# Kernel tuning notes

Hardware: AMD Instinct MI355X
Metric: run time of the kernel (lower is better)

The kernel has to match this reference:

```python
import jax, jax.numpy as jnp
import numpy as np

WEIGHT = 0.1  # HISCLoss weight


def _gram(X):
    # linear kernel (the module's 'rbf' branch computes X @ Y.T)
    X = X.reshape(X.shape[0], -1)
    return X @ X.T  # [B, B]


def _center(K):
    # H K H with H = I - 11^T/B  ==  K - rowmean - colmean + grandmean
    rm = K.mean(axis=1, keepdims=True)
    cm = K.mean(axis=0, keepdims=True)
    gm = K.mean()
    return K - rm - cm + gm


def _hsic(X, Y):
    B = X.shape[0]
    Kc = _center(_gram(X))
    Lc = _center(_gram(Y))
    # trace(Kc @ Lc) without the B^3 matmul
    tr = jnp.einsum('ij,ji->', Kc, Lc)
    return tr / ((B - 1) ** 2)


def setup_inputs() -> dict:
    key = jax.random.key(0)
    ks = jax.random.split(key, 4)
    B, d = 4096, 256
    return {
        'e0': jax.random.normal(ks[0], (B, d), dtype=jnp.float32),
        'e1': jax.random.normal(ks[1], (B, d), dtype=jnp.float32),
        'e2': jax.random.normal(ks[2], (B, d), dtype=jnp.float32),
        'e3': jax.random.normal(ks[3], (B, d), dtype=jnp.float32),
    }


def reference(e0, e1, e2, e3):
    experts = [e0, e1, e2, e3]
    n = len(experts)
    vals = []
    for i in range(n):
        for j in range(i + 1, n):
            vals.append(_hsic(experts[i], experts[j]))
    L_hsic = jnp.mean(jnp.stack(vals))
    return WEIGHT * L_hsic
```

## Files before the change

### kernel.cpp

```cpp
#include <hip/hip_runtime.h>
#include <hip/hip_bf16.h>

#define B_ROWS 4096
#define DIM 256
#define NPAIR 6
#define PITCH 4160
#define BK 256
#define KSPLIT 8
#define KCHUNK (B_ROWS / KSPLIT)

typedef short bf16x8 __attribute__((ext_vector_type(8)));
typedef float f32x4 __attribute__((ext_vector_type(4)));

__device__ __forceinline__ const float* sel(const float* e0, const float* e1,
                                            const float* e2, const float* e3, int i) {
    return i == 0 ? e0 : (i == 1 ? e1 : (i == 2 ? e2 : e3));
}

__device__ __forceinline__ int pair_i(int p) { return p < 3 ? 0 : (p < 5 ? 1 : 2); }
__device__ __forceinline__ int pair_j(int p) { return p < 3 ? p + 1 : (p < 5 ? p - 1 : 3); }

__device__ __forceinline__ unsigned short f32_to_bf16_rne(float f) {
    unsigned int u = __float_as_uint(f);
    unsigned int r = (u + 0x7FFFu + ((u >> 16) & 1u)) >> 16;
    return (unsigned short)r;
}

__device__ __forceinline__ void glds16(const void* g, void* l) {
    __builtin_amdgcn_global_load_lds(
        (const __attribute__((address_space(1))) unsigned int*)(g),
        (__attribute__((address_space(3))) unsigned int*)(l), 16, 0, 0);
}


__global__ __launch_bounds__(256) void transpose_bf16_kernel(
        const float* __restrict__ e0, const float* __restrict__ e1,
        const float* __restrict__ e2, const float* __restrict__ e3,
        unsigned short* __restrict__ XT, float* __restrict__ sums_p) {
    int rt = blockIdx.x;
    int ct = blockIdx.y;
    int e  = blockIdx.z;
    const float* X = sel(e0, e1, e2, e3, e);
    unsigned short* XTe = XT + (size_t)e * DIM * PITCH;

    __shared__ float T[64][65];

    int t = threadIdx.x;
    int c4 = (t & 15) << 2;
    #pragma unroll
    for (int p = 0; p < 4; ++p) {
        int r = (t >> 4) + 16 * p;
        float4 v = *(const float4*)&X[(size_t)(rt * 64 + r) * DIM + ct * 64 + c4];
        T[c4 + 0][r] = v.x;
        T[c4 + 1][r] = v.y;
        T[c4 + 2][r] = v.z;
        T[c4 + 3][r] = v.w;
    }
    __syncthreads();

    #pragma unroll
    for (int p = 0; p < 2; ++p) {
        int id = 256 * p + t;
        int c = id >> 3;
        int roff = (id & 7) * 8;
        bf16x8 outv;
        float s8 = 0.f;
        #pragma unroll
        for (int s = 0; s < 8; ++s) {
            float f = T[c][roff + s];
            outv[s] = (short)f32_to_bf16_rne(f);
            s8 += f;
        }
        *(bf16x8*)&XTe[(size_t)(ct * 64 + c) * PITCH + rt * 64 + roff] = outv;
        s8 += __shfl_down(s8, 4, 8);
        s8 += __shfl_down(s8, 2, 8);
        s8 += __shfl_down(s8, 1, 8);
        if ((id & 7) == 0)
            sums_p[((size_t)(e * DIM + ct * 64 + c)) * 64 + rt] = s8;
    }
}

__global__ __launch_bounds__(512) void gram_v8_kernel(
        const unsigned short* __restrict__ XT, const float* __restrict__ sums_p,
        float* __restrict__ part) {
    __shared__ __align__(16) unsigned short smem[2 * 64 * 256];
    char* base = (char*)smem;

    int blk = blockIdx.x;
    int p = blk >> 6;
    int tile = blk & 63;
    int a0 = (tile >> 3) * 32;
    int b0 = (tile & 7) * 32;
    int pi = pair_i(p), pj = pair_j(p);
    const unsigned short* Xp = XT + (size_t)pi * DIM * PITCH;
    const unsigned short* Yp = XT + (size_t)pj * DIM * PITCH;

    int tid = threadIdx.x;
    int w = tid >> 6;
    int L = tid & 63;

    int srow = tid >> 5;
    int soffb = (tid & 31) * 16;
    int swzb = soffb ^ ((srow & 7) << 4);
    const unsigned short* gA0 = Xp + (size_t)(a0 + srow) * PITCH + (swzb >> 1);
    const unsigned short* gA1 = Xp + (size_t)(a0 + 16 + srow) * PITCH + (swzb >> 1);
    const unsigned short* gB0 = Yp + (size_t)(b0 + srow) * PITCH + (swzb >> 1);
    const unsigned short* gB1 = Yp + (size_t)(b0 + 16 + srow) * PITCH + (swzb >> 1);
    int lp0 = tid * 16;
    int lp1 = 8192 + tid * 16;

    int rA = L & 15;
    int koffb = w * 64 + (L >> 4) * 16;
    int fr0 = rA * 512 + (koffb ^ ((rA & 7) << 4));

    f32x4 acc[2][2] = {};

    glds16(gA0, base + lp0);
    glds16(gA1, base + lp1);
    glds16(gB0, base + 16384 + lp0);
    glds16(gB1, base + 16384 + lp1);
    __syncthreads();

    for (int c = 0; c < 16; ++c) {
        if (c < 15) {
            int cn = (c + 1) * BK;
            char* Ab = base + ((c + 1) & 1) * 32768;
            glds16(gA0 + cn, Ab + lp0);
            glds16(gA1 + cn, Ab + lp1);
            glds16(gB0 + cn, Ab + 16384 + lp0);
            glds16(gB1 + cn, Ab + 16384 + lp1);
        }
        const char* Ar = base + (c & 1) * 32768;
        bf16x8 a0f = *(const bf16x8*)(Ar + fr0);
        bf16x8 a1f = *(const bf16x8*)(Ar + 8192 + fr0);
        bf16x8 b0f = *(const bf16x8*)(Ar + 16384 + fr0);
        bf16x8 b1f = *(const bf16x8*)(Ar + 16384 + 8192 + fr0);
        acc[0][0] = __builtin_amdgcn_mfma_f32_16x16x32_bf16(a0f, b0f, acc[0][0], 0, 0, 0);
        acc[0][1] = __builtin_amdgcn_mfma_f32_16x16x32_bf16(a0f, b1f, acc[0][1], 0, 0, 0);
        acc[1][0] = __builtin_amdgcn_mfma_f32_16x16x32_bf16(a1f, b0f, acc[1][0], 0, 0, 0);
        acc[1][1] = __builtin_amdgcn_mfma_f32_16x16x32_bf16(a1f, b1f, acc[1][1], 0, 0, 0);
        __syncthreads();
    }

    float* red  = (float*)base;
    float* sA   = (float*)(base + 33792);
    float* sB   = (float*)(base + 33920);
    float* wsum = (float*)(base + 34048);

    #pragma unroll
    for (int ti = 0; ti < 2; ++ti)
        #pragma unroll
        for (int tj = 0; tj < 2; ++tj)
            #pragma unroll
            for (int r = 0; r < 4; ++r) {
                int m = ti * 16 + (L >> 4) * 4 + r;
                int n = tj * 16 + (L & 15);
                red[w * 1056 + m * 33 + n] = acc[ti][tj][r];
            }

    {
        int fl = tid >> 4;
        int pr = tid & 15;
        float4 va = *(const float4*)&sums_p[((size_t)(pi * DIM + a0 + fl)) * 64 + pr * 4];
        float4 vb = *(const float4*)&sums_p[((size_t)(pj * DIM + b0 + fl)) * 64 + pr * 4];
        float sa = va.x + va.y + va.z + va.w;
        float sb = vb.x + vb.y + vb.z + vb.w;
        sa += __shfl_down(sa, 8, 16);
        sa += __shfl_down(sa, 4, 16);
        sa += __shfl_down(sa, 2, 16);
        sa += __shfl_down(sa, 1, 16);
        sb += __shfl_down(sb, 8, 16);
        sb += __shfl_down(sb, 4, 16);
        sb += __shfl_down(sb, 2, 16);
        sb += __shfl_down(sb, 1, 16);
        if (pr == 0) { sA[fl] = sa; sB[fl] = sb; }
    }
    __syncthreads();

    const float inv_b = 1.0f / (float)B_ROWS;
    float local = 0.f;
    #pragma unroll
    for (int q = 0; q < 2; ++q) {
        int pos = tid + q * 512;
        int m = pos >> 5, n = pos & 31;
        float s = 0.f;
        #pragma unroll
        for (int ww = 0; ww < 8; ++ww) s += red[ww * 1056 + m * 33 + n];
        float v = s - sA[m] * sB[n] * inv_b;
        local = fmaf(v, v, local);
    }
    #pragma unroll
    for (int off = 32; off > 0; off >>= 1) local += __shfl_down(local, off, 64);
    if (L == 0) wsum[w] = local;
    __syncthreads();
    if (tid == 0) {
        float s = 0.f;
        #pragma unroll
        for (int ww = 0; ww < 8; ++ww) s += wsum[ww];
        part[blk] = s;
    }
}

__global__ __launch_bounds__(512) void finalize384_kernel(
        const float* __restrict__ part, float* __restrict__ out) {
    int t = threadIdx.x;
    float local = (t < NPAIR * 64) ? part[t] : 0.f;
    #pragma unroll
    for (int off = 32; off > 0; off >>= 1) local += __shfl_down(local, off, 64);
    __shared__ float ws2[8];
    if ((t & 63) == 0) ws2[t >> 6] = local;
    __syncthreads();
    if (t == 0) {
        float s = 0.f;
        #pragma unroll
        for (int ww = 0; ww < 8; ++ww) s += ws2[ww];
        const float scale = 0.1f / (6.0f * 4095.0f * 4095.0f);
        out[0] = s * scale;
    }
}

__global__ void finalize_kernel(const float* __restrict__ acc, float* __restrict__ out) {
    if (threadIdx.x == 0) {
        const float scale = 0.1f / (6.0f * 4095.0f * 4095.0f);
        out[0] = acc[0] * scale;
    }
}


__global__ void col_sums_kernel(const float* __restrict__ e0, const float* __restrict__ e1,
                                const float* __restrict__ e2, const float* __restrict__ e3,
                                float* __restrict__ sums) {
    int e = blockIdx.y;
    const float* X = sel(e0, e1, e2, e3, e);
    int c = threadIdx.x;
    int r0 = blockIdx.x * 128;
    float s = 0.f;
    #pragma unroll 4
    for (int r = r0; r < r0 + 128; ++r) s += X[r * DIM + c];
    atomicAdd(&sums[e * DIM + c], s);
}

__global__ __launch_bounds__(256) void gram_kernel(
        const float* __restrict__ e0, const float* __restrict__ e1,
        const float* __restrict__ e2, const float* __restrict__ e3,
        float* __restrict__ G) {
    int kc = blockIdx.x;
    int tile = blockIdx.y;
    int p = blockIdx.z;
    const float* X = sel(e0, e1, e2, e3, pair_i(p));
    const float* Y = sel(e0, e1, e2, e3, pair_j(p));
    int a0 = (tile >> 2) * 64;
    int b0 = (tile & 3) * 64;
    int k0 = kc * KCHUNK;
    __shared__ float As[16][64];
    __shared__ float Bs[16][64];
    int lid = threadIdx.x;
    int lr = lid >> 4;
    int lc = (lid & 15) << 2;
    int ty = lid >> 4;
    int tx = lid & 15;
    float acc[4][4] = {};
    for (int ks = 0; ks < KCHUNK; ks += 16) {
        int row = k0 + ks + lr;
        float4 av = *(const float4*)&X[row * DIM + a0 + lc];
        float4 bv = *(const float4*)&Y[row * DIM + b0 + lc];
        __syncthreads();
        *(float4*)&As[lr][lc] = av;
        *(float4*)&Bs[lr][lc] = bv;
        __syncthreads();
        #pragma unroll
        for (int k = 0; k < 16; ++k) {
            float a[4], b[4];
            *(float4*)a = *(const float4*)&As[k][ty * 4];
            *(float4*)b = *(const float4*)&Bs[k][tx * 4];
            #pragma unroll
            for (int i = 0; i < 4; ++i)
                #pragma unroll
                for (int j = 0; j < 4; ++j)
                    acc[i][j] = fmaf(a[i], b[j], acc[i][j]);
        }
    }
    float* Gp = G + p * (DIM * DIM);
    #pragma unroll
    for (int i = 0; i < 4; ++i)
        #pragma unroll
        for (int j = 0; j < 4; ++j)
            atomicAdd(&Gp[(a0 + ty * 4 + i) * DIM + (b0 + tx * 4 + j)], acc[i][j]);
}

__global__ void reduce_kernel(const float* __restrict__ G, const float* __restrict__ sums,
                              float* __restrict__ acc) {
    float local = 0.f;
    const int total = NPAIR * DIM * DIM;
    for (int idx = blockIdx.x * blockDim.x + threadIdx.x; idx < total;
         idx += gridDim.x * blockDim.x) {
        int p = idx >> 16;
        int ab = idx & 65535;
        int a = ab >> 8;
        int b = ab & 255;
        float v = G[idx] - sums[pair_i(p) * DIM + a] * sums[pair_j(p) * DIM + b] * (1.0f / (float)B_ROWS);
        local = fmaf(v, v, local);
    }
    #pragma unroll
    for (int off = 32; off > 0; off >>= 1) local += __shfl_down(local, off, 64);
    __shared__ float wsum[4];
    if ((threadIdx.x & 63) == 0) wsum[threadIdx.x >> 6] = local;
    __syncthreads();
    if (threadIdx.x == 0) {
        float s = wsum[0] + wsum[1] + wsum[2] + wsum[3];
        atomicAdd(acc, s);
    }
}


extern "C" void kernel_launch(void* const* d_in, const int* in_sizes, int n_in,
                              void* d_out, int out_size, void* d_ws, size_t ws_size,
                              hipStream_t stream) {
    const float* e0 = (const float*)d_in[0];
    const float* e1 = (const float*)d_in[1];
    const float* e2 = (const float*)d_in[2];
    const float* e3 = (const float*)d_in[3];

    size_t need = 266240 + (size_t)4 * DIM * PITCH * sizeof(unsigned short);

    if (ws_size >= need) {
        float* sums_p = (float*)d_ws;
        float* part = (float*)((char*)d_ws + 262144);
        unsigned short* XT = (unsigned short*)((char*)d_ws + 266240);
        transpose_bf16_kernel<<<dim3(64, 4, 4), 256, 0, stream>>>(e0, e1, e2, e3, XT, sums_p);
        gram_v8_kernel<<<NPAIR * 64, 512, 0, stream>>>(XT, sums_p, part);
        finalize384_kernel<<<1, 512, 0, stream>>>(part, (float*)d_out);
    } else {
        float* sums = (float*)d_ws;
        float* acc  = (float*)((char*)d_ws + 4096);
        float* G = (float*)((char*)d_ws + 8192);
        size_t zbytes = 8192 + (size_t)NPAIR * DIM * DIM * sizeof(float);
        hipMemsetAsync(d_ws, 0, zbytes, stream);
        col_sums_kernel<<<dim3(32, 4), 256, 0, stream>>>(e0, e1, e2, e3, sums);
        gram_kernel<<<dim3(KSPLIT, 16, NPAIR), 256, 0, stream>>>(e0, e1, e2, e3, G);
        reduce_kernel<<<384, 256, 0, stream>>>(G, sums, acc);
        finalize_kernel<<<1, 64, 0, stream>>>(acc, (float*)d_out);
    }
}
```

Measured before the change: 85.29 us.

## Fuse transpose, gram and finalize into one cooperative kernel with grid syncs

```diff
diff --git a/kernel.cpp b/kernel.cpp
--- a/kernel.cpp
+++ b/kernel.cpp
@@ -1,5 +1,8 @@
 #include <hip/hip_runtime.h>
 #include <hip/hip_bf16.h>
+#include <hip/hip_cooperative_groups.h>
+
+namespace cg = cooperative_groups;
 
 #define B_ROWS 4096
 #define DIM 256
@@ -30,6 +33,193 @@
     __builtin_amdgcn_global_load_lds(
         (const __attribute__((address_space(1))) unsigned int*)(g),
         (__attribute__((address_space(3))) unsigned int*)(l), 16, 0, 0);
+}
+
+__global__ __launch_bounds__(512, 4) void fused_kernel(
+        const float* __restrict__ e0, const float* __restrict__ e1,
+        const float* __restrict__ e2, const float* __restrict__ e3,
+        unsigned short* __restrict__ XT, float* __restrict__ sums_p,
+        float* __restrict__ part, float* __restrict__ out) {
+    __shared__ __align__(16) char smem[65536];
+    int blk = blockIdx.x;
+    int tid = threadIdx.x;
+
+    {
+        float (*T)[65] = (float(*)[65])smem;
+        for (int task = blk; task < 1024; task += 384) {
+            int rt = task & 63;
+            int ct = (task >> 6) & 3;
+            int e  = task >> 8;
+            const float* X = sel(e0, e1, e2, e3, e);
+            unsigned short* XTe = XT + (size_t)e * DIM * PITCH;
+
+            int c4 = (tid & 15) << 2;
+            #pragma unroll
+            for (int p = 0; p < 2; ++p) {
+                int r = (tid >> 4) + 32 * p;
+                float4 v = *(const float4*)&X[(size_t)(rt * 64 + r) * DIM + ct * 64 + c4];
+                T[c4 + 0][r] = v.x;
+                T[c4 + 1][r] = v.y;
+                T[c4 + 2][r] = v.z;
+                T[c4 + 3][r] = v.w;
+            }
+            __syncthreads();
+
+            int c = tid >> 3;
+            int roff = (tid & 7) * 8;
+            bf16x8 outv;
+            float s8 = 0.f;
+            #pragma unroll
+            for (int s = 0; s < 8; ++s) {
+                float f = T[c][roff + s];
+                outv[s] = (short)f32_to_bf16_rne(f);
+                s8 += f;
+            }
+            *(bf16x8*)&XTe[(size_t)(ct * 64 + c) * PITCH + rt * 64 + roff] = outv;
+            s8 += __shfl_down(s8, 4, 8);
+            s8 += __shfl_down(s8, 2, 8);
+            s8 += __shfl_down(s8, 1, 8);
+            if ((tid & 7) == 0)
+                sums_p[((size_t)(e * DIM + ct * 64 + c)) * 64 + rt] = s8;
+            __syncthreads();
+        }
+    }
+
+    __threadfence();
+    cg::this_grid().sync();
+
+    char* base = smem;
+    int p = blk >> 6;
+    int tile = blk & 63;
+    int a0 = (tile >> 3) * 32;
+    int b0 = (tile & 7) * 32;
+    int pi = pair_i(p), pj = pair_j(p);
+    const unsigned short* Xp = XT + (size_t)pi * DIM * PITCH;
+    const unsigned short* Yp = XT + (size_t)pj * DIM * PITCH;
+
+    int w = tid >> 6;
+    int L = tid & 63;
+
+    int srow = tid >> 5;
+    int soffb = (tid & 31) * 16;
+    int swzb = soffb ^ ((srow & 7) << 4);
+    const unsigned short* gA0 = Xp + (size_t)(a0 + srow) * PITCH + (swzb >> 1);
+    const unsigned short* gA1 = Xp + (size_t)(a0 + 16 + srow) * PITCH + (swzb >> 1);
+    const unsigned short* gB0 = Yp + (size_t)(b0 + srow) * PITCH + (swzb >> 1);
+    const unsigned short* gB1 = Yp + (size_t)(b0 + 16 + srow) * PITCH + (swzb >> 1);
+    int lp0 = tid * 16;
+    int lp1 = 8192 + tid * 16;
+
+    int rA = L & 15;
+    int koffb = w * 64 + (L >> 4) * 16;
+    int fr0 = rA * 512 + (koffb ^ ((rA & 7) << 4));
+
+    f32x4 acc[2][2] = {};
+
+    glds16(gA0, base + lp0);
+    glds16(gA1, base + lp1);
+    glds16(gB0, base + 16384 + lp0);
+    glds16(gB1, base + 16384 + lp1);
+    __syncthreads();
+
+    for (int c = 0; c < 16; ++c) {
+        if (c < 15) {
+            int cn = (c + 1) * BK;
+            char* Ab = base + ((c + 1) & 1) * 32768;
+            glds16(gA0 + cn, Ab + lp0);
+            glds16(gA1 + cn, Ab + lp1);
+            glds16(gB0 + cn, Ab + 16384 + lp0);
+            glds16(gB1 + cn, Ab + 16384 + lp1);
+        }
+        const char* Ar = base + (c & 1) * 32768;
+        bf16x8 a0f = *(const bf16x8*)(Ar + fr0);
+        bf16x8 a1f = *(const bf16x8*)(Ar + 8192 + fr0);
+        bf16x8 b0f = *(const bf16x8*)(Ar + 16384 + fr0);
+        bf16x8 b1f = *(const bf16x8*)(Ar + 16384 + 8192 + fr0);
+        acc[0][0] = __builtin_amdgcn_mfma_f32_16x16x32_bf16(a0f, b0f, acc[0][0], 0, 0, 0);
+        acc[0][1] = __builtin_amdgcn_mfma_f32_16x16x32_bf16(a0f, b1f, acc[0][1], 0, 0, 0);
+        acc[1][0] = __builtin_amdgcn_mfma_f32_16x16x32_bf16(a1f, b0f, acc[1][0], 0, 0, 0);
+        acc[1][1] = __builtin_amdgcn_mfma_f32_16x16x32_bf16(a1f, b1f, acc[1][1], 0, 0, 0);
+        __syncthreads();
+    }
+
+    float* red  = (float*)base;
+    float* sA   = (float*)(base + 33792);
+    float* sB   = (float*)(base + 33920);
+    float* wsum = (float*)(base + 34048);
+
+    #pragma unroll
+    for (int ti = 0; ti < 2; ++ti)
+        #pragma unroll
+        for (int tj = 0; tj < 2; ++tj)
+            #pragma unroll
+            for (int r = 0; r < 4; ++r) {
+                int m = ti * 16 + (L >> 4) * 4 + r;
+                int n = tj * 16 + (L & 15);
+                red[w * 1056 + m * 33 + n] = acc[ti][tj][r];
+            }
+
+    {
+        int fl = tid >> 4;
+        int pr = tid & 15;
+        float4 va = *(const float4*)&sums_p[((size_t)(pi * DIM + a0 + fl)) * 64 + pr * 4];
+        float4 vb = *(const float4*)&sums_p[((size_t)(pj * DIM + b0 + fl)) * 64 + pr * 4];
+        float sa = va.x + va.y + va.z + va.w;
+        float sb = vb.x + vb.y + vb.z + vb.w;
+        sa += __shfl_down(sa, 8, 16);
+        sa += __shfl_down(sa, 4, 16);
+        sa += __shfl_down(sa, 2, 16);
+        sa += __shfl_down(sa, 1, 16);
+        sb += __shfl_down(sb, 8, 16);
+        sb += __shfl_down(sb, 4, 16);
+        sb += __shfl_down(sb, 2, 16);
+        sb += __shfl_down(sb, 1, 16);
+        if (pr == 0) { sA[fl] = sa; sB[fl] = sb; }
+    }
+    __syncthreads();
+
+    const float inv_b = 1.0f / (float)B_ROWS;
+    float local = 0.f;
+    #pragma unroll
+    for (int q = 0; q < 2; ++q) {
+        int pos = tid + q * 512;
+        int m = pos >> 5, n = pos & 31;
+        float s = 0.f;
+        #pragma unroll
+        for (int ww = 0; ww < 8; ++ww) s += red[ww * 1056 + m * 33 + n];
+        float v = s - sA[m] * sB[n] * inv_b;
+        local = fmaf(v, v, local);
+    }
+    #pragma unroll
+    for (int off = 32; off > 0; off >>= 1) local += __shfl_down(local, off, 64);
+    if (L == 0) wsum[w] = local;
+    __syncthreads();
+    if (tid == 0) {
+        float s = 0.f;
+        #pragma unroll
+        for (int ww = 0; ww < 8; ++ww) s += wsum[ww];
+        part[blk] = s;
+    }
+
+    __threadfence();
+    cg::this_grid().sync();
+
+    if (blk == 0) {
+        float local3 = (tid < NPAIR * 64) ? part[tid] : 0.f;
+        #pragma unroll
+        for (int off = 32; off > 0; off >>= 1) local3 += __shfl_down(local3, off, 64);
+        float* ws2 = (float*)base;
+        __syncthreads();
+        if ((tid & 63) == 0) ws2[tid >> 6] = local3;
+        __syncthreads();
+        if (tid == 0) {
+            float s = 0.f;
+            #pragma unroll
+            for (int ww = 0; ww < 8; ++ww) s += ws2[ww];
+            const float scale = 0.1f / (6.0f * 4095.0f * 4095.0f);
+            out[0] = s * scale;
+        }
+    }
 }
 
 
@@ -327,9 +517,17 @@
         float* sums_p = (float*)d_ws;
         float* part = (float*)((char*)d_ws + 262144);
         unsigned short* XT = (unsigned short*)((char*)d_ws + 266240);
-        transpose_bf16_kernel<<<dim3(64, 4, 4), 256, 0, stream>>>(e0, e1, e2, e3, XT, sums_p);
-        gram_v8_kernel<<<NPAIR * 64, 512, 0, stream>>>(XT, sums_p, part);
-        finalize384_kernel<<<1, 512, 0, stream>>>(part, (float*)d_out);
+        float* outp = (float*)d_out;
+
+        void* args[] = {(void*)&e0, (void*)&e1, (void*)&e2, (void*)&e3,
+                        (void*)&XT, (void*)&sums_p, (void*)&part, (void*)&outp};
+        hipError_t err = hipLaunchCooperativeKernel(
+            (const void*)fused_kernel, dim3(NPAIR * 64), dim3(512), args, 0, stream);
+        if (err != hipSuccess) {
+            transpose_bf16_kernel<<<dim3(64, 4, 4), 256, 0, stream>>>(e0, e1, e2, e3, XT, sums_p);
+            gram_v8_kernel<<<NPAIR * 64, 512, 0, stream>>>(XT, sums_p, part);
+            finalize384_kernel<<<1, 512, 0, stream>>>(part, (float*)d_out);
+        }
     } else {
         float* sums = (float*)d_ws;
         float* acc  = (float*)((char*)d_ws + 4096);
```

After: 295.6 us. +246.6%, slower.
